# Kernel optimization log

Hardware: AMD Instinct MI355X
Metric: run time of the kernel (lower is better)

The kernel has to match this reference:

```python
import jax, jax.numpy as jnp
import numpy as np

B, D, H, O = 8192, 512, 16384, 1000

def _row_normalize(w):
    return w / jnp.linalg.norm(w, axis=1, keepdims=True)

def setup_inputs() -> dict:
    key = jax.random.key(0)
    k0, k1, k2, k3 = jax.random.split(key, 4)
    x = jax.random.normal(k0, (B, D), dtype=jnp.float32)
    kohonen_weights = _row_normalize(jax.random.normal(k1, (H, D), dtype=jnp.float32))
    G_fwd = _row_normalize(jax.random.normal(k2, (O, H), dtype=jnp.float32))
    G_rev = _row_normalize(jax.random.normal(k3, (D, H), dtype=jnp.float32))
    return {"x": x, "kohonen_weights": kohonen_weights, "G_fwd": G_fwd, "G_rev": G_rev}

def reference(x, kohonen_weights, G_fwd, G_rev):
    # torch.cdist(x, W): Euclidean distances, shape (B, H).
    x2 = jnp.sum(x * x, axis=1, keepdims=True)          # (B, 1)
    w2 = jnp.sum(kohonen_weights * kohonen_weights, axis=1)  # (H,)
    d2 = x2 - 2.0 * (x @ kohonen_weights.T) + w2[None, :]    # (B, H)
    distances = jnp.sqrt(jnp.maximum(d2, 0.0))
    winners = jnp.argmin(distances, axis=1)              # (B,)
    # one_hot @ G_fwd.T == gather of G_fwd columns (same math, no dense GEMM)
    output = G_fwd.T[winners]                            # (B, O)
    recos = G_rev.T[winners]                             # (B, D)
    return (output, recos, winners)
```

## Files before the change

kernel.cpp:

```cpp
#include <hip/hip_runtime.h>
#include <stdint.h>

constexpr int kB = 8192;
constexpr int kD = 512;
constexpr int kH = 16384;
constexpr int kO = 1000;
constexpr int kNB64 = kH / 64;
constexpr float kMargin = 0.055f;

typedef _Float16 half8v __attribute__((ext_vector_type(8)));
typedef _Float16 half4v __attribute__((ext_vector_type(4)));
typedef float float4v __attribute__((ext_vector_type(4)));

#define VMW(n) asm volatile("s_waitcnt vmcnt(" #n ")" ::: "memory")

constexpr size_t OFF_XH  = 0;
constexpr size_t OFF_WH  = OFF_XH + (size_t)kB * kD * 2;
constexpr size_t OFF_W2  = OFF_WH + (size_t)kH * kD * 2;
constexpr size_t OFF_BT  = OFF_W2 + 65536;
constexpr size_t OFF_GFT = OFF_BT + (size_t)kB * kNB64 * 8;
constexpr size_t OFF_GRT = OFF_GFT + (size_t)kH * kO * 4;
constexpr size_t WS_NEED = OFF_GRT + (size_t)kH * kD * 4;

__device__ inline unsigned mono32(float s) {
    unsigned u = __float_as_uint(s);
    return u ^ ((u & 0x80000000u) ? 0xFFFFFFFFu : 0x80000000u);
}
__device__ inline float dq32(unsigned key) {
    unsigned u = key & 0xFFFFFFC0u;
    u ^= (u & 0x80000000u) ? 0x80000000u : 0xFFFFFFFFu;
    return __uint_as_float(u);
}
__device__ inline unsigned long long packkey(float s, int h) {
    return ((unsigned long long)mono32(s) << 32) | (unsigned)h;
}
__device__ inline unsigned long long u64min(unsigned long long a, unsigned long long b) {
    return a < b ? a : b;
}

template <typename T>
__device__ inline void gload_lds16(const T* g, T* l) {
    __builtin_amdgcn_global_load_lds(
        (const __attribute__((address_space(1))) uint32_t*)g,
        (__attribute__((address_space(3))) uint32_t*)l, 16, 0, 0);
}

__global__ __launch_bounds__(256) void prep_kernel(const float* __restrict__ x,
                                                   const float* __restrict__ W,
                                                   _Float16* __restrict__ xh,
                                                   _Float16* __restrict__ wh,
                                                   float* __restrict__ w2) {
    if (blockIdx.x < 2048) {
        size_t i = (size_t)blockIdx.x * 256 + threadIdx.x;
        const float4* s4 = reinterpret_cast<const float4*>(x);
        float4 a = s4[i * 2], b = s4[i * 2 + 1];
        half8v h = {(_Float16)a.x, (_Float16)a.y, (_Float16)a.z, (_Float16)a.w,
                    (_Float16)b.x, (_Float16)b.y, (_Float16)b.z, (_Float16)b.w};
        *reinterpret_cast<half8v*>(xh + i * 8) = h;
    } else {
        int bx = blockIdx.x - 2048;
        int lane = threadIdx.x & 63;
        int wv   = threadIdx.x >> 6;
        int row  = bx * 4 + wv;
        const float4* Wr = reinterpret_cast<const float4*>(W + (size_t)row * kD);
        float s = 0.f;
#pragma unroll
        for (int i = 0; i < 2; ++i) {
            float4 v = Wr[lane + i * 64];
            s += v.x * v.x + v.y * v.y + v.z * v.z + v.w * v.w;
            half4v h = {(_Float16)v.x, (_Float16)v.y, (_Float16)v.z, (_Float16)v.w};
            *reinterpret_cast<half4v*>(wh + (size_t)row * kD + i * 256 + lane * 4) = h;
        }
#pragma unroll
        for (int off = 32; off; off >>= 1) s += __shfl_xor(s, off, 64);
        if (lane == 0) w2[row] = s;
    }
}

__global__ __launch_bounds__(256) void transpose2_kernel(const float* __restrict__ Gf,
                                                         float* __restrict__ GfT,
                                                         const float* __restrict__ Gr,
                                                         float* __restrict__ GrT,
                                                         int useTf, int useTr) {
    const float* src; float* dst; int R, r0;
    if (blockIdx.y < 32) {
        if (!useTf) return;
        src = Gf; dst = GfT; R = kO; r0 = blockIdx.y * 32;
    } else {
        if (!useTr) return;
        src = Gr; dst = GrT; R = kD; r0 = (blockIdx.y - 32) * 32;
    }
    const int C = kH;
    __shared__ float s[32][33];
    const int tx = threadIdx.x & 31;
    const int ty = threadIdx.x >> 5;
    const int c0 = blockIdx.x * 32;
#pragma unroll
    for (int i = 0; i < 4; ++i) {
        int r = r0 + ty + i * 8;
        if (r < R) s[ty + i * 8][tx] = src[(size_t)r * C + c0 + tx];
    }
    __syncthreads();
#pragma unroll
    for (int i = 0; i < 4; ++i) {
        int c = c0 + ty + i * 8;
        if (r0 + tx < R) dst[(size_t)c * R + r0 + tx] = s[tx][ty + i * 8];
    }
}

__global__ __launch_bounds__(512, 2) void gemm_argmin_mfma(
    const _Float16* __restrict__ xh, const _Float16* __restrict__ wh,
    const float* __restrict__ w2, uint2* __restrict__ blocktop)
{
    __shared__ __align__(16) _Float16 sm[65536];

    const int tid  = threadIdx.x;
    const int lane = tid & 63;
    const int wv   = tid >> 6;
    const int wr   = wv >> 2;
    const int wc   = wv & 3;

    int bid = blockIdx.x;
    int swz = (bid & 7) * (2048 / 8) + (bid >> 3);
    const int hb  = swz & 63;
    const int mb  = swz >> 6;
    const int bm0 = mb * 256, hn0 = hb * 256;

    float4v acc[8][4];
#pragma unroll
    for (int i = 0; i < 8; ++i)
#pragma unroll
        for (int j = 0; j < 4; ++j) acc[i][j] = (float4v){0.f, 0.f, 0.f, 0.f};

    auto STAGEH = [&](int h) {
        const int T2 = h >> 2, jp = h & 3;
        const int kk = jp >> 1, isB = jp & 1;
        const int kt = T2 * 64 + kk * 32;
        _Float16* dst0 = &sm[(((T2 & 1) << 2) | jp) * 8192 + wv * 512];
#pragma unroll
        for (int l = 0; l < 2; ++l) {
            const int idx = l * 512 + tid;
            const int r = idx >> 2, c = idx & 3;
            const int sc = c ^ ((r >> 1) & 3);
            const _Float16* src =
                (isB ? wh + (size_t)(hn0 + r) * kD : xh + (size_t)(bm0 + r) * kD)
                + kt + sc * 8;
            gload_lds16(src, dst0 + l * 4096);
        }
    };

    auto PH2 = [&](int buf, int kk, int q) {
        const int fbase = buf * 32768 + kk * 16384;
        half8v bfr[4], afr[8];
#pragma unroll
        for (int jn = 0; jn < 4; ++jn) {
            const int r = wc * 64 + jn * 16 + (lane & 15);
            const int cs = (lane >> 4) ^ ((r >> 1) & 3);
            bfr[jn] = *reinterpret_cast<const half8v*>(&sm[fbase + 8192 + r * 32 + cs * 8]);
        }
#pragma unroll
        for (int im = 0; im < 8; ++im) {
            const int r = wr * 128 + im * 16 + (lane & 15);
            const int cs = (lane >> 4) ^ ((r >> 1) & 3);
            afr[im] = *reinterpret_cast<const half8v*>(&sm[fbase + r * 32 + cs * 8]);
        }
        if (q < 16) {
            const int h = 4 * (q >> 1) + 2 * (q & 1);
            STAGEH(h);
            STAGEH(h + 1);
        }
        __builtin_amdgcn_s_barrier();
        asm volatile("s_waitcnt lgkmcnt(0)" ::: "memory");
        __builtin_amdgcn_sched_barrier(0);
        __builtin_amdgcn_s_setprio(1);
#pragma unroll
        for (int im = 0; im < 8; ++im)
#pragma unroll
            for (int jn = 0; jn < 4; ++jn)
                acc[im][jn] =
                    __builtin_amdgcn_mfma_f32_16x16x32_f16(afr[im], bfr[jn],
                                                           acc[im][jn], 0, 0, 0);
        __builtin_amdgcn_s_setprio(0);
    };

    STAGEH(0); STAGEH(1);
    STAGEH(2); STAGEH(3);
    STAGEH(4); STAGEH(5);
    VMW(4);
    __builtin_amdgcn_s_barrier();

    PH2(0, 0, 3);           __builtin_amdgcn_s_barrier();
    PH2(0, 1, 4);  VMW(4);  __builtin_amdgcn_s_barrier();
    PH2(1, 0, 5);           __builtin_amdgcn_s_barrier();
    PH2(1, 1, 6);  VMW(4);  __builtin_amdgcn_s_barrier();
    PH2(0, 0, 7);           __builtin_amdgcn_s_barrier();
    PH2(0, 1, 8);  VMW(4);  __builtin_amdgcn_s_barrier();
    PH2(1, 0, 9);           __builtin_amdgcn_s_barrier();
    PH2(1, 1, 10); VMW(4);  __builtin_amdgcn_s_barrier();
    PH2(0, 0, 11);          __builtin_amdgcn_s_barrier();
    PH2(0, 1, 12); VMW(4);  __builtin_amdgcn_s_barrier();
    PH2(1, 0, 13);          __builtin_amdgcn_s_barrier();
    PH2(1, 1, 14); VMW(4);  __builtin_amdgcn_s_barrier();
    PH2(0, 0, 15);          __builtin_amdgcn_s_barrier();
    PH2(0, 1, 16); VMW(4);  __builtin_amdgcn_s_barrier();
    PH2(1, 0, 16); VMW(0);  __builtin_amdgcn_s_barrier();
    PH2(1, 1, 16);

    float w2v[4];
#pragma unroll
    for (int j = 0; j < 4; ++j) w2v[j] = w2[hn0 + wc * 64 + j * 16 + (lane & 15)];

#pragma unroll
    for (int i = 0; i < 8; ++i) {
#pragma unroll
        for (int r = 0; r < 4; ++r) {
            unsigned k1 = 0xFFFFFFFFu, k2 = 0xFFFFFFFFu;
#pragma unroll
            for (int j = 0; j < 4; ++j) {
                float s = fmaf(-2.f, acc[i][j][r], w2v[j]);
                unsigned key = (mono32(s) & 0xFFFFFFC0u)
                             | (unsigned)(j * 16 + (lane & 15));
                if (key < k1) { k2 = k1; k1 = key; }
                else if (key < k2) { k2 = key; }
            }
#pragma unroll
            for (int m = 1; m < 16; m <<= 1) {
                unsigned o1 = (unsigned)__shfl_xor((int)k1, m, 64);
                unsigned o2 = (unsigned)__shfl_xor((int)k2, m, 64);
                unsigned n1 = min(k1, o1);
                unsigned mx = max(k1, o1);
                k2 = min(min(k2, o2), mx);
                k1 = n1;
            }
            if ((lane & 15) == 0) {
                int rl = wr * 128 + i * 16 + (lane >> 4) * 4 + r;
                blocktop[(size_t)(bm0 + rl) * kNB64 + hb * 4 + wc] =
                    (uint2){k1, k2};
            }
        }
    }
}

__global__ __launch_bounds__(256) void finish_kernel(
    const float* __restrict__ x, const float* __restrict__ W,
    const float* __restrict__ w2, const uint2* __restrict__ blocktop,
    const float* __restrict__ Gf, const float* __restrict__ Gr,
    const float* __restrict__ GfT, const float* __restrict__ GrT,
    int useTf, int useTr, float* __restrict__ out)
{
    const int tid = threadIdx.x;
    const int b = blockIdx.x;
    __shared__ float xs[kD];
    __shared__ unsigned long long red[256];
    __shared__ unsigned long long sv1, sv2;
    __shared__ int clist[kNB64];
    __shared__ int ccount;

    if (tid < 128)
        reinterpret_cast<float4*>(xs)[tid] =
            reinterpret_cast<const float4*>(x + (size_t)b * kD)[tid];
    if (tid == 0) ccount = 0;

    uint2 t12 = blocktop[(size_t)b * kNB64 + tid];

    red[tid] = ((unsigned long long)t12.x << 8) | (unsigned)tid;
    __syncthreads();
    for (int s = 128; s > 0; s >>= 1) {
        if (tid < s) red[tid] = u64min(red[tid], red[tid + s]);
        __syncthreads();
    }
    if (tid == 0) sv1 = red[0];
    __syncthreads();
    const unsigned long long v1k = sv1;
    const int b1hb = (int)(v1k & 0xFFu);
    const unsigned v1key = (unsigned)(v1k >> 8);
    const float v1s = dq32(v1key);
    const int v1h = b1hb * 64 + (int)(v1key & 63u);

    red[tid] = ((unsigned long long)((tid == b1hb) ? t12.y : t12.x) << 8) | (unsigned)tid;
    __syncthreads();
    for (int s = 128; s > 0; s >>= 1) {
        if (tid < s) red[tid] = u64min(red[tid], red[tid + s]);
        __syncthreads();
    }
    if (tid == 0) sv2 = red[0];
    __syncthreads();
    const float v2s = dq32((unsigned)(sv2 >> 8));

    int idx;
    if (v2s - v1s > kMargin) {
        idx = v1h;
    } else {
        if (dq32(t12.x) <= v1s + kMargin) {
            int p = atomicAdd(&ccount, 1);
            clist[p] = tid;
        }
        __syncthreads();
        const int nc = ccount;
        const int wvf = tid >> 6, lnf = tid & 63;
        unsigned long long bestk = ~0ull;
        for (int c = wvf; c < nc; c += 4) {
            int h = clist[c] * 64 + lnf;
            const float4* wr = reinterpret_cast<const float4*>(W + (size_t)h * kD);
            float dot = 0.f;
            for (int k = 0; k < kD / 4; ++k) {
                float4 wvv = wr[k];
                dot = fmaf(xs[k * 4 + 0], wvv.x, dot);
                dot = fmaf(xs[k * 4 + 1], wvv.y, dot);
                dot = fmaf(xs[k * 4 + 2], wvv.z, dot);
                dot = fmaf(xs[k * 4 + 3], wvv.w, dot);
            }
            float s = fmaf(-2.f, dot, w2[h]);
            bestk = u64min(bestk, packkey(s, h));
        }
        red[tid] = bestk;
        __syncthreads();
        for (int s = 128; s > 0; s >>= 1) {
            if (tid < s) red[tid] = u64min(red[tid], red[tid + s]);
            __syncthreads();
        }
        idx = (int)(unsigned)(red[0] & 0xFFFFFFFFu);
    }

    float* out0 = out;
    float* out1 = out + (size_t)kB * kO;
    float* outw = out + (size_t)kB * (kO + kD);
    if (useTf) {
        const float4* gfr = reinterpret_cast<const float4*>(GfT + (size_t)idx * kO);
        float4* o0 = reinterpret_cast<float4*>(out0 + (size_t)b * kO);
        for (int o = tid; o < kO / 4; o += 256) o0[o] = gfr[o];
    } else {
        for (int o = tid; o < kO; o += 256)
            out0[(size_t)b * kO + o] = Gf[(size_t)o * kH + idx];
    }
    if (useTr) {
        const float4* grr = reinterpret_cast<const float4*>(GrT + (size_t)idx * kD);
        float4* o1 = reinterpret_cast<float4*>(out1 + (size_t)b * kD);
        if (tid < kD / 4) o1[tid] = grr[tid];
    } else {
        for (int d = tid; d < kD; d += 256)
            out1[(size_t)b * kD + d] = Gr[(size_t)d * kH + idx];
    }
    if (tid == 0) outw[b] = (float)idx;
}

extern "C" void kernel_launch(void* const* d_in, const int* in_sizes, int n_in,
                              void* d_out, int out_size, void* d_ws, size_t ws_size,
                              hipStream_t stream) {
    const float* x  = (const float*)d_in[0];
    const float* W  = (const float*)d_in[1];
    const float* Gf = (const float*)d_in[2];
    const float* Gr = (const float*)d_in[3];
    float* out = (float*)d_out;

    char* ws = (char*)d_ws;
    _Float16* xh = (_Float16*)(ws + OFF_XH);
    _Float16* wh = (_Float16*)(ws + OFF_WH);
    float* w2 = (float*)(ws + OFF_W2);
    uint2* blocktop = (uint2*)(ws + OFF_BT);
    float* GfT = (float*)(ws + OFF_GFT);
    float* GrT = (float*)(ws + OFF_GRT);
    const int useTf = (ws_size >= OFF_GRT) ? 1 : 0;
    const int useTr = (ws_size >= WS_NEED) ? 1 : 0;

    hipLaunchKernelGGL(prep_kernel, dim3(2048 + 4096), dim3(256), 0, stream,
                       x, W, xh, wh, w2);
    if (useTf || useTr)
        hipLaunchKernelGGL(transpose2_kernel, dim3(kH / 32, 48), dim3(256), 0, stream,
                           Gf, GfT, Gr, GrT, useTf, useTr);
    hipLaunchKernelGGL(gemm_argmin_mfma, dim3(2048), dim3(512), 0, stream,
                       xh, wh, w2, blocktop);
    hipLaunchKernelGGL(finish_kernel, dim3(kB), dim3(256), 0, stream,
                       x, W, w2, blocktop, Gf, Gr, GfT, GrT, useTf, useTr, out);
}
```

Before: 324.8 us.

## Restructure GEMM main loop to a one-tile-ahead double buffer with one barrier per tile

Replaces the hand-unrolled schedule of half-tile phases, which had a barrier after every phase and partial vmcnt waits, with a loop over K tiles. Each tile's two halves run back to back while the next tile is staged into the other LDS buffer, and there is a single full vmcnt wait plus barrier per tile. The prologue now stages only the first tile. This halves barrier count and simplifies sync, but shortens the prefetch distance, so global loads have less time to land before they are needed.

```diff
diff --git a/kernel.cpp b/kernel.cpp
--- a/kernel.cpp
+++ b/kernel.cpp
@@ -149,7 +149,7 @@
         }
     };
 
-    auto PH2 = [&](int buf, int kk, int q) {
+    auto HALF = [&](int buf, int kk, int hstage) {
         const int fbase = buf * 32768 + kk * 16384;
         half8v bfr[4], afr[8];
 #pragma unroll
@@ -164,12 +164,10 @@
             const int cs = (lane >> 4) ^ ((r >> 1) & 3);
             afr[im] = *reinterpret_cast<const half8v*>(&sm[fbase + r * 32 + cs * 8]);
         }
-        if (q < 16) {
-            const int h = 4 * (q >> 1) + 2 * (q & 1);
-            STAGEH(h);
-            STAGEH(h + 1);
-        }
-        __builtin_amdgcn_s_barrier();
+        if (hstage >= 0) {
+            STAGEH(hstage);
+            STAGEH(hstage + 1);
+        }
         asm volatile("s_waitcnt lgkmcnt(0)" ::: "memory");
         __builtin_amdgcn_sched_barrier(0);
         __builtin_amdgcn_s_setprio(1);
@@ -183,28 +181,21 @@
         __builtin_amdgcn_s_setprio(0);
     };
 
-    STAGEH(0); STAGEH(1);
-    STAGEH(2); STAGEH(3);
-    STAGEH(4); STAGEH(5);
-    VMW(4);
+    STAGEH(0); STAGEH(1); STAGEH(2); STAGEH(3);
+    VMW(0);
     __builtin_amdgcn_s_barrier();
 
-    PH2(0, 0, 3);           __builtin_amdgcn_s_barrier();
-    PH2(0, 1, 4);  VMW(4);  __builtin_amdgcn_s_barrier();
-    PH2(1, 0, 5);           __builtin_amdgcn_s_barrier();
-    PH2(1, 1, 6);  VMW(4);  __builtin_amdgcn_s_barrier();
-    PH2(0, 0, 7);           __builtin_amdgcn_s_barrier();
-    PH2(0, 1, 8);  VMW(4);  __builtin_amdgcn_s_barrier();
-    PH2(1, 0, 9);           __builtin_amdgcn_s_barrier();
-    PH2(1, 1, 10); VMW(4);  __builtin_amdgcn_s_barrier();
-    PH2(0, 0, 11);          __builtin_amdgcn_s_barrier();
-    PH2(0, 1, 12); VMW(4);  __builtin_amdgcn_s_barrier();
-    PH2(1, 0, 13);          __builtin_amdgcn_s_barrier();
-    PH2(1, 1, 14); VMW(4);  __builtin_amdgcn_s_barrier();
-    PH2(0, 0, 15);          __builtin_amdgcn_s_barrier();
-    PH2(0, 1, 16); VMW(4);  __builtin_amdgcn_s_barrier();
-    PH2(1, 0, 16); VMW(0);  __builtin_amdgcn_s_barrier();
-    PH2(1, 1, 16);
+#pragma unroll
+    for (int T = 0; T < 8; ++T) {
+        const int buf = T & 1;
+        const int hs = (T < 7) ? 4 * (T + 1) : -2;
+        HALF(buf, 0, hs);
+        HALF(buf, 1, hs >= 0 ? hs + 2 : -2);
+        if (T < 7) {
+            VMW(0);
+            __builtin_amdgcn_s_barrier();
+        }
+    }
 
     float w2v[4];
 #pragma unroll
```

New measurement: 318.3 us. 2.0% less time.
